# Performance work log

Hardware: AMD Instinct MI355X
Metric: run time of the kernel (lower is better)

The kernel has to match this reference:

```python
import jax, jax.numpy as jnp
import numpy as np

NUM_CLASSES = 2048
FEAT_DIM = 512
BATCH = 8192


def setup_inputs() -> dict:
    key = jax.random.key(0)
    k1, k2, k3 = jax.random.split(key, 3)
    features = jax.random.normal(k1, (BATCH, FEAT_DIM), dtype=jnp.float32)
    centers = jax.random.normal(k2, (NUM_CLASSES, FEAT_DIM), dtype=jnp.float32)
    target = jax.random.randint(k3, (BATCH,), 0, NUM_CLASSES, dtype=jnp.int64)
    return {"features": features, "centers": centers, "target": target}


def reference(features, centers, target):
    batch_size = features.shape[0]
    # distmat[i, j] = ||f_i||^2 + ||c_j||^2 - 2 f_i . c_j  (matches addmm_ with beta=1, alpha=-2)
    f_sq = jnp.sum(features * features, axis=1, keepdims=True)        # [N, 1]
    c_sq = jnp.sum(centers * centers, axis=1)[None, :]                # [1, C]
    distmat = f_sq + c_sq - 2.0 * jnp.einsum('nd,cd->nc', features, centers)
    # one-hot mask of target class per row
    classes = jnp.arange(NUM_CLASSES)
    mask = (target[:, None] == classes[None, :]).astype(distmat.dtype)  # [N, C]
    dist = distmat * mask
    loss = jnp.clip(dist, 1e-12, 1.0e12).sum() / batch_size
    return loss
```

## Files before the change

kernel.cpp:

```cpp
#include <hip/hip_runtime.h>

#define BATCH 8192
#define FEAT_DIM 512
#define NUM_CLASSES 2048

#define WAVES_PER_BLOCK 4
#define BLOCKS1 (BATCH / WAVES_PER_BLOCK)

__global__ __launch_bounds__(256)
void center_loss_partial(const float* __restrict__ features,
                         const float* __restrict__ centers,
                         const int* __restrict__ target,
                         float* __restrict__ ws) {
    const int wave = threadIdx.x >> 6;
    const int lane = threadIdx.x & 63;
    const int row  = blockIdx.x * WAVES_PER_BLOCK + wave;

    const int t = target[row];
    const float4* __restrict__ fp =
        (const float4*)(features + (size_t)row * FEAT_DIM);
    const float4* __restrict__ cp =
        (const float4*)(centers + (size_t)t * FEAT_DIM);

    const float4 a0 = fp[lane];
    const float4 a1 = fp[lane + 64];
    const float4 b0 = cp[lane];
    const float4 b1 = cp[lane + 64];

    const float dx0 = a0.x - b0.x, dy0 = a0.y - b0.y;
    const float dz0 = a0.z - b0.z, dw0 = a0.w - b0.w;
    const float dx1 = a1.x - b1.x, dy1 = a1.y - b1.y;
    const float dz1 = a1.z - b1.z, dw1 = a1.w - b1.w;
    float acc = dx0 * dx0 + dy0 * dy0 + dz0 * dz0 + dw0 * dw0
              + dx1 * dx1 + dy1 * dy1 + dz1 * dz1 + dw1 * dw1;

#pragma unroll
    for (int off = 32; off > 0; off >>= 1)
        acc += __shfl_xor(acc, off, 64);

    if (lane == 0)
        ws[row] = fminf(fmaxf(acc, 1e-12f), 1.0e12f);
}

__global__ __launch_bounds__(256)
void center_loss_final(const float4* __restrict__ ws, float* __restrict__ out) {
    const int tid  = threadIdx.x;
    const int wave = tid >> 6;
    const int lane = tid & 63;

    float acc = 0.0f;
#pragma unroll
    for (int i = 0; i < 8; ++i) {
        const float4 v = ws[tid + 256 * i];
        acc += (v.x + v.y) + (v.z + v.w);
    }

#pragma unroll
    for (int off = 32; off > 0; off >>= 1)
        acc += __shfl_xor(acc, off, 64);

    __shared__ float s[4];
    if (lane == 0) s[wave] = acc;
    __syncthreads();
    if (tid == 0) {
        const float total = (s[0] + s[1]) + (s[2] + s[3]);
        out[0] = total * (1.0f / (float)BATCH)
               + (float)(NUM_CLASSES - 1) * 1e-12f;
    }
}

extern "C" void kernel_launch(void* const* d_in, const int* in_sizes, int n_in,
                              void* d_out, int out_size, void* d_ws, size_t ws_size,
                              hipStream_t stream) {
    const float* features = (const float*)d_in[0];
    const float* centers  = (const float*)d_in[1];
    const int*   target   = (const int*)d_in[2];
    float* out = (float*)d_out;
    float* ws  = (float*)d_ws;

    center_loss_partial<<<BLOCKS1, 256, 0, stream>>>(features, centers, target, ws);
    center_loss_final<<<1, 256, 0, stream>>>((const float4*)ws, out);
}
```

Baseline: 11.49 us.

## Fuse final reduction into main kernel via hierarchical fixed-point atomic counters

Replaces the two-kernel partial/final reduction with one kernel. Each block sums its four rows, converts the sum to fixed point and adds it to one of 64 padded slots with a 64-bit atomic. The low 8 bits of each slot count arrivals, so the last block in a group forwards the group sum to a global slot, and the last group writes the result. This removes the second kernel launch and the workspace round trip, but adds a hipMemsetAsync before each launch plus atomic traffic, and it quantizes the sum to fixed point.

```diff
diff --git a/kernel.cpp b/kernel.cpp
--- a/kernel.cpp
+++ b/kernel.cpp
@@ -5,13 +5,19 @@
 #define NUM_CLASSES 2048
 
 #define WAVES_PER_BLOCK 4
-#define BLOCKS1 (BATCH / WAVES_PER_BLOCK)
+#define NBLOCKS (BATCH / WAVES_PER_BLOCK)
+#define NSLOTS 64
+#define GROUP_SZ (NBLOCKS / NSLOTS)
+#define SLOT_STRIDE 32
+#define SCALE 268435456.0
+
 
 __global__ __launch_bounds__(256)
-void center_loss_partial(const float* __restrict__ features,
-                         const float* __restrict__ centers,
-                         const int* __restrict__ target,
-                         float* __restrict__ ws) {
+void center_loss_fused(const float* __restrict__ features,
+                       const float* __restrict__ centers,
+                       const int* __restrict__ target,
+                       unsigned long long* __restrict__ slots,
+                       float* __restrict__ out) {
     const int wave = threadIdx.x >> 6;
     const int lane = threadIdx.x & 63;
     const int row  = blockIdx.x * WAVES_PER_BLOCK + wave;
@@ -38,34 +44,36 @@
     for (int off = 32; off > 0; off >>= 1)
         acc += __shfl_xor(acc, off, 64);
 
+    __shared__ float s[WAVES_PER_BLOCK];
     if (lane == 0)
-        ws[row] = fminf(fmaxf(acc, 1e-12f), 1.0e12f);
-}
+        s[wave] = fminf(fmaxf(acc, 1e-12f), 1.0e12f);
+    __syncthreads();
 
-__global__ __launch_bounds__(256)
-void center_loss_final(const float4* __restrict__ ws, float* __restrict__ out) {
-    const int tid  = threadIdx.x;
-    const int wave = tid >> 6;
-    const int lane = tid & 63;
+    if (threadIdx.x == 0) {
+        const float bsum = (s[0] + s[1]) + (s[2] + s[3]);
 
-    float acc = 0.0f;
-#pragma unroll
-    for (int i = 0; i < 8; ++i) {
-        const float4 v = ws[tid + 256 * i];
-        acc += (v.x + v.y) + (v.z + v.w);
-    }
+        const unsigned long long q =
+            (unsigned long long)((double)bsum * SCALE);
+        const unsigned long long inc = (q << 8) | 1ull;
 
-#pragma unroll
-    for (int off = 32; off > 0; off >>= 1)
-        acc += __shfl_xor(acc, off, 64);
+        const int g = blockIdx.x & (NSLOTS - 1);
+        const unsigned long long old1 =
+            atomicAdd(&slots[g * SLOT_STRIDE], inc);
+        const unsigned long long v1 = old1 + inc;
 
-    __shared__ float s[4];
-    if (lane == 0) s[wave] = acc;
-    __syncthreads();
-    if (tid == 0) {
-        const float total = (s[0] + s[1]) + (s[2] + s[3]);
-        out[0] = total * (1.0f / (float)BATCH)
-               + (float)(NUM_CLASSES - 1) * 1e-12f;
+        if ((v1 & 0xFFull) == (unsigned long long)GROUP_SZ) {
+            const unsigned long long sg = v1 >> 8;
+            const unsigned long long inc2 = (sg << 8) | 1ull;
+            const unsigned long long old2 =
+                atomicAdd(&slots[NSLOTS * SLOT_STRIDE], inc2);
+            const unsigned long long v2 = old2 + inc2;
+
+            if ((v2 & 0xFFull) == (unsigned long long)NSLOTS) {
+                const double total = (double)(v2 >> 8) * (1.0 / SCALE);
+                out[0] = (float)(total * (1.0 / (double)BATCH)
+                                 + (double)(NUM_CLASSES - 1) * 1e-12);
+            }
+        }
     }
 }
 
@@ -76,8 +84,12 @@
     const float* centers  = (const float*)d_in[1];
     const int*   target   = (const int*)d_in[2];
     float* out = (float*)d_out;
-    float* ws  = (float*)d_ws;
+    unsigned long long* slots = (unsigned long long*)d_ws;
 
-    center_loss_partial<<<BLOCKS1, 256, 0, stream>>>(features, centers, target, ws);
-    center_loss_final<<<1, 256, 0, stream>>>((const float4*)ws, out);
+    hipMemsetAsync(slots, 0,
+                   (NSLOTS * SLOT_STRIDE + 1) * sizeof(unsigned long long),
+                   stream);
+
+    center_loss_fused<<<NBLOCKS, 256, 0, stream>>>(features, centers, target,
+                                                   slots, out);
 }
```

New measurement: 15.47 us. 1.35x slower.
